# Kernel tuning notes

Measured on AMD Instinct MI355X. Metric: run time of the kernel, lower is better.

The kernel has to match this reference:

```python
import jax, jax.numpy as jnp
import numpy as np

B, K, D = 8, 256, 768      # batch, num proposals, appearance_feature_dim
DK = 96                    # key_feature_dim
DG = 96                    # geo_feature_dim
NR = 8                     # n_relations (NR*DK == D required by residual add)


def setup_inputs() -> dict:
    key = jax.random.key(0)
    ks = jax.random.split(key, 10)
    s = 0.02
    return {
        "f_a": jax.random.normal(ks[0], (B, K, D), jnp.float32),
        "position_embedding": jax.random.uniform(ks[1], (B, K, K, DG), jnp.float32),
        # stacked per-head parameters (NR heads)
        "WG_w": jax.random.normal(ks[2], (NR, DG), jnp.float32) * s,
        "WG_b": jnp.zeros((NR,), jnp.float32),
        "WK_w": jax.random.normal(ks[3], (NR, D, DK), jnp.float32) * s,
        "WK_b": jnp.zeros((NR, DK), jnp.float32),
        "WQ_w": jax.random.normal(ks[4], (NR, D, DK), jnp.float32) * s,
        "WQ_b": jnp.zeros((NR, DK), jnp.float32),
        "WV_w": jax.random.normal(ks[5], (NR, D, DK), jnp.float32) * s,
        "WV_b": jnp.zeros((NR, DK), jnp.float32),
    }


def reference(f_a, position_embedding, WG_w, WG_b, WK_w, WK_b, WQ_w, WQ_b, WV_w, WV_b):
    # Per-head projections, all heads at once: [B, H, K, DK]
    k = jnp.einsum('bkd,hde->bhke', f_a, WK_w) + WK_b[:, None, :]
    q = jnp.einsum('bkd,hde->bhke', f_a, WQ_w) + WQ_b[:, None, :]
    v = jnp.einsum('bkd,hde->bhke', f_a, WV_w) + WV_b[:, None, :]
    # scaled_dot[b,h,m,n] = <k_m, q_n> / sqrt(DK)  (matches w_k.view(B,K,1,dk)*w_q.view(B,1,K,dk))
    scores = jnp.einsum('bhme,bhne->bhmn', k, q) * (1.0 / np.sqrt(DK)).astype(np.float32)
    # geometric bias: relu(WG(pe)) -> [B,H,K,K]
    w_g = jax.nn.relu(jnp.einsum('bmng,hg->bhmn', position_embedding, WG_w) + WG_b[:, None, None])
    logits = jnp.log(jnp.clip(w_g, 1e-6)) + scores
    # torch Softmax(dim=1) on [B,K,K] -> normalize over m axis (axis=2 here)
    attn = jax.nn.softmax(logits, axis=2)
    # output[b,n,:] = sum_m attn[b,h,m,n] * v[b,h,m,:], heads concatenated on feature dim
    out = jnp.einsum('bhmn,bhmd->bnhd', attn, v).reshape(f_a.shape[0], f_a.shape[1], -1)
    return out + f_a  # concat + f_a residual from RelationalProposalModule
```

## Files before the change

kernel.cpp:

```cpp
#include <hip/hip_runtime.h>

#define DD   768
#define NH   8
#define DKh  96

typedef __attribute__((ext_vector_type(8))) short short8;
typedef __attribute__((ext_vector_type(4))) float f32x4;

__device__ __forceinline__ unsigned short f2bf(float x) {
    union { float f; unsigned int u; } v; v.f = x;
    unsigned int r = v.u + 0x7FFFu + ((v.u >> 16) & 1u);
    return (unsigned short)(r >> 16);
}

__global__ __launch_bounds__(256) void k_cvt_a(const float* __restrict__ fa,
                                               unsigned short* __restrict__ abf) {
    int idx = blockIdx.x * 256 + threadIdx.x;
    float4 v = ((const float4*)fa)[idx];
    ushort4 o;
    o.x = f2bf(v.x); o.y = f2bf(v.y); o.z = f2bf(v.z); o.w = f2bf(v.w);
    ((ushort4*)abf)[idx] = o;
}

__global__ __launch_bounds__(256) void k_cvt_w(const float* __restrict__ wk,
                                               const float* __restrict__ wq,
                                               const float* __restrict__ wv,
                                               unsigned short* __restrict__ wbf) {
    __shared__ float ls[64 * 97];
    int pid = blockIdx.x / 12;
    int db  = blockIdx.x % 12;
    int p = pid >> 3, h = pid & 7;
    const float* src = (p == 0 ? wk : p == 1 ? wq : wv) + h * DD * DKh + db * 64 * DKh;
    int t = threadIdx.x;
#pragma unroll
    for (int i = 0; i < 24; ++i) {
        int f = t + 256 * i;
        int dl = f / 96, e = f - dl * 96;
        ls[dl * 97 + e] = src[f];
    }
    __syncthreads();
    unsigned short* dst = wbf + (p * 768 + h * 96) * DD + db * 64;
#pragma unroll
    for (int i = 0; i < 24; ++i) {
        int f = t + 256 * i;
        int e = f >> 6, dl = f & 63;
        dst[e * DD + dl] = f2bf(ls[dl * 97 + e]);
    }
}

__global__ __launch_bounds__(256) void k_proj(const unsigned short* __restrict__ abf,
                                              const unsigned short* __restrict__ wbf,
                                              const float* __restrict__ wkb,
                                              const float* __restrict__ wqb,
                                              const float* __restrict__ wvb,
                                              unsigned short* __restrict__ kb,
                                              unsigned short* __restrict__ qb,
                                              unsigned short* __restrict__ vt) {
    int w = threadIdx.x >> 6, lane = threadIdx.x & 63;
    int lrow = lane & 15, quad = lane >> 4;
    int rt = blockIdx.x / 36, cg = blockIdx.x % 36;
    int r0 = rt * 64 + w * 16;
    int c0 = cg * 64;
    f32x4 z = {0.f, 0.f, 0.f, 0.f};
    f32x4 acc[4] = {z, z, z, z};
    for (int kk = 0; kk < DD; kk += 32) {
        short8 a = *(const short8*)(abf + (r0 + lrow) * DD + kk + quad * 8);
#pragma unroll
        for (int tt = 0; tt < 4; ++tt) {
            short8 b = *(const short8*)(wbf + (c0 + tt * 16 + lrow) * DD + kk + quad * 8);
            acc[tt] = __builtin_amdgcn_mfma_f32_16x16x32_bf16(a, b, acc[tt], 0, 0, 0);
        }
    }
    int rbase = r0 + quad * 4;
    int b_ = rbase >> 8, mbase = rbase & 255;
#pragma unroll
    for (int tt = 0; tt < 4; ++tt) {
        int cc = c0 + tt * 16 + lrow;
        int p = cc / 768, rm = cc - p * 768;
        int h = rm / 96,  e = rm - h * 96;
        float bias = (p == 0 ? wkb : p == 1 ? wqb : wvb)[h * 96 + e];
        if (p == 2) {
            ushort4 v4;
            v4.x = f2bf(acc[tt][0] + bias);
            v4.y = f2bf(acc[tt][1] + bias);
            v4.z = f2bf(acc[tt][2] + bias);
            v4.w = f2bf(acc[tt][3] + bias);
            *(ushort4*)(vt + ((b_ * 8 + h) * 96 + e) * 256 + mbase) = v4;
        } else {
            float sc = (p == 1) ? 0.10206207261596577f : 1.0f;
            unsigned short* dst = (p == 0 ? kb : qb) + ((b_ * 8 + h) * 256 + mbase) * 96 + e;
#pragma unroll
            for (int r = 0; r < 4; ++r)
                dst[r * 96] = f2bf((acc[tt][r] + bias) * sc);
        }
    }
}

__global__ __launch_bounds__(256) void k_wgs(const float* __restrict__ pe,
                                             const float* __restrict__ wgw,
                                             const float* __restrict__ wgb,
                                             const unsigned short* __restrict__ kb,
                                             const unsigned short* __restrict__ qb,
                                             float* __restrict__ L) {
    __shared__ unsigned short peb[256 * 96];
    __shared__ unsigned short wgl[16 * 96];
    __shared__ float stot[8 * 256];
    int bi = blockIdx.x;
    int b = bi >> 8, mt = (bi >> 4) & 15, nt = bi & 15;
    int m0 = mt * 16, n0 = nt * 16;
    int t = threadIdx.x;
#pragma unroll
    for (int i = 0; i < 6; ++i) {
        int f = t + 256 * i;
        int c = f / 96, k = f - c * 96;
        wgl[f] = (c < 8) ? f2bf(wgw[c * 96 + k]) : (unsigned short)0;
    }
    const float* peg = pe + ((size_t)(b * 256 + m0) * 256 + n0) * 96;
#pragma unroll
    for (int i = 0; i < 24; ++i) {
        int f = t + 256 * i;
        int mi = f / 384, rem = f - mi * 384;
        float4 v = *(const float4*)(peg + (size_t)mi * 24576 + rem * 4);
        ushort4 o;
        o.x = f2bf(v.x); o.y = f2bf(v.y); o.z = f2bf(v.z); o.w = f2bf(v.w);
        *(ushort4*)(peb + mi * 1536 + rem * 4) = o;
    }
    __syncthreads();
    int w = t >> 6, lane = t & 63, lrow = lane & 15, quad = lane >> 4;
    short8 bf[3];
#pragma unroll
    for (int ks = 0; ks < 3; ++ks)
        bf[ks] = *(const short8*)(wgl + lrow * 96 + ks * 32 + quad * 8);
    float gbias = wgb[lrow & 7];
#pragma unroll
    for (int rt4 = 0; rt4 < 4; ++rt4) {
        int rt = w * 4 + rt4;
        f32x4 acc = {0.f, 0.f, 0.f, 0.f};
#pragma unroll
        for (int ks = 0; ks < 3; ++ks) {
            short8 a = *(const short8*)(peb + (rt * 16 + lrow) * 96 + ks * 32 + quad * 8);
            acc = __builtin_amdgcn_mfma_f32_16x16x32_bf16(a, bf[ks], acc, 0, 0, 0);
        }
        if (lrow < 8) {
#pragma unroll
            for (int r = 0; r < 4; ++r)
                stot[lrow * 256 + rt * 16 + quad * 4 + r] =
                    __logf(fmaxf(acc[r] + gbias, 1e-6f));
        }
    }
    __syncthreads();
#pragma unroll
    for (int hh = 0; hh < 2; ++hh) {
        int h = w * 2 + hh;
        const unsigned short* ka = kb + ((size_t)((b * 8 + h) * 256) + m0 + lrow) * 96 + quad * 8;
        const unsigned short* qa = qb + ((size_t)((b * 8 + h) * 256) + n0 + lrow) * 96 + quad * 8;
        f32x4 acc = {0.f, 0.f, 0.f, 0.f};
#pragma unroll
        for (int ks = 0; ks < 3; ++ks) {
            short8 a  = *(const short8*)(ka + ks * 32);
            short8 bq = *(const short8*)(qa + ks * 32);
            acc = __builtin_amdgcn_mfma_f32_16x16x32_bf16(a, bq, acc, 0, 0, 0);
        }
        float* lp = L + ((size_t)((b * 8 + h) * 256) + m0 + quad * 4) * 256 + n0 + lrow;
#pragma unroll
        for (int r = 0; r < 4; ++r)
            lp[r * 256] = acc[r] + stot[h * 256 + (quad * 4 + r) * 16 + lrow];
    }
}

__global__ __launch_bounds__(256) void k_softmax(const float* __restrict__ L,
                                                 unsigned short* __restrict__ pt) {
    __shared__ float Ps[32 * 264];
    __shared__ float inv_s[32];
    int bh = blockIdx.x >> 3, nbk = blockIdx.x & 7;
    int n0 = nbk * 32;
    int t = threadIdx.x;
    int nl = t >> 3, j = t & 7;
    const float* base = L + bh * 65536 + n0 + nl;
    float mx = -3.4e38f;
    for (int m0 = 0; m0 < 256; m0 += 8)
        mx = fmaxf(mx, base[(m0 + j) * 256]);
    mx = fmaxf(mx, __shfl_xor(mx, 1));
    mx = fmaxf(mx, __shfl_xor(mx, 2));
    mx = fmaxf(mx, __shfl_xor(mx, 4));
    float sum = 0.f;
    for (int m0 = 0; m0 < 256; m0 += 8) {
        float v = base[(m0 + j) * 256];
        float e = __expf(v - mx);
        sum += e;
        Ps[nl * 264 + m0 + j] = e;
    }
    sum += __shfl_xor(sum, 1);
    sum += __shfl_xor(sum, 2);
    sum += __shfl_xor(sum, 4);
    if (j == 0) inv_s[nl] = 1.0f / sum;
    __syncthreads();
    unsigned short* dst = pt + (bh * 256 + n0) * 256;
#pragma unroll 4
    for (int i = 0; i < 32; ++i)
        dst[i * 256 + t] = f2bf(Ps[i * 264 + t] * inv_s[i]);
}

__global__ __launch_bounds__(256) void k_attnv(const unsigned short* __restrict__ pt,
                                               const unsigned short* __restrict__ vt,
                                               const float* __restrict__ fa,
                                               float* __restrict__ out) {
    int w = threadIdx.x >> 6, lane = threadIdx.x & 63;
    int lrow = lane & 15, quad = lane >> 4;
    int tid = blockIdx.x * 4 + w;
    int bh = tid / 96, rem = tid - bh * 96;
    int nt = rem / 6, et = rem - nt * 6;
    int n0 = nt * 16, e0 = et * 16;
    int b_ = bh >> 3, h = bh & 7;
    f32x4 acc = {0.f, 0.f, 0.f, 0.f};
    const unsigned short* pa = pt + (bh * 256 + n0 + lrow) * 256 + quad * 8;
    const unsigned short* va = vt + (bh * 96 + e0 + lrow) * 256 + quad * 8;
#pragma unroll
    for (int mk = 0; mk < 256; mk += 32) {
        short8 a = *(const short8*)(pa + mk);
        short8 b = *(const short8*)(va + mk);
        acc = __builtin_amdgcn_mfma_f32_16x16x32_bf16(a, b, acc, 0, 0, 0);
    }
    int idx = (b_ * 256 + n0 + quad * 4) * 768 + h * 96 + e0 + lrow;
#pragma unroll
    for (int r = 0; r < 4; ++r)
        out[idx + r * 768] = acc[r] + fa[idx + r * 768];
}

extern "C" void kernel_launch(void* const* d_in, const int* in_sizes, int n_in,
                              void* d_out, int out_size, void* d_ws, size_t ws_size,
                              hipStream_t stream) {
    const float* fa  = (const float*)d_in[0];
    const float* pe  = (const float*)d_in[1];
    const float* wgw = (const float*)d_in[2];
    const float* wgb = (const float*)d_in[3];
    const float* wkw = (const float*)d_in[4];
    const float* wkb = (const float*)d_in[5];
    const float* wqw = (const float*)d_in[6];
    const float* wqb = (const float*)d_in[7];
    const float* wvw = (const float*)d_in[8];
    const float* wvb = (const float*)d_in[9];
    float* out = (float*)d_out;
    char* ws = (char*)d_ws;
    unsigned short* abf = (unsigned short*)(ws);
    unsigned short* wbf = (unsigned short*)(ws + 3145728);
    unsigned short* kb  = (unsigned short*)(ws + 6684672);
    unsigned short* qb  = (unsigned short*)(ws + 9830400);
    unsigned short* vt  = (unsigned short*)(ws + 12976128);
    float*          L   = (float*)(ws + 16121856);
    unsigned short* pt  = (unsigned short*)(ws + 32899072);

    k_cvt_a  <<<1536, 256, 0, stream>>>(fa, abf);
    k_cvt_w  <<< 288, 256, 0, stream>>>(wkw, wqw, wvw, wbf);
    k_proj   <<<1152, 256, 0, stream>>>(abf, wbf, wkb, wqb, wvb, kb, qb, vt);
    k_wgs    <<<2048, 256, 0, stream>>>(pe, wgw, wgb, kb, qb, L);
    k_softmax<<< 512, 256, 0, stream>>>(L, pt);
    k_attnv  <<<1536, 256, 0, stream>>>(pt, vt, fa, out);
}
```

Baseline: 404.7 us.

## Fuse softmax with attn-V, transpose logits layout, merge conversion kernels

The two conversion kernels are merged into one launch. k_wgs now writes the logits transposed (n-major, m contiguous) with vectorized float4 stores, so the softmax over m becomes a contiguous row reduction using wave shuffles. Softmax and the attention-times-V product are fused into one kernel that keeps normalized probabilities in LDS as bf16, removing the pt round trip through global memory and two launches. The fused kernel launches only 512 blocks, which may lower parallelism in the matmul phase.

After: 390.7 us. -3.4%, faster.

```diff
diff --git a/kernel.cpp b/kernel.cpp
--- a/kernel.cpp
+++ b/kernel.cpp
@@ -13,25 +13,28 @@
     return (unsigned short)(r >> 16);
 }
 
-__global__ __launch_bounds__(256) void k_cvt_a(const float* __restrict__ fa,
-                                               unsigned short* __restrict__ abf) {
-    int idx = blockIdx.x * 256 + threadIdx.x;
-    float4 v = ((const float4*)fa)[idx];
-    ushort4 o;
-    o.x = f2bf(v.x); o.y = f2bf(v.y); o.z = f2bf(v.z); o.w = f2bf(v.w);
-    ((ushort4*)abf)[idx] = o;
-}
-
-__global__ __launch_bounds__(256) void k_cvt_w(const float* __restrict__ wk,
-                                               const float* __restrict__ wq,
-                                               const float* __restrict__ wv,
-                                               unsigned short* __restrict__ wbf) {
+__global__ __launch_bounds__(256) void k_cvt(const float* __restrict__ fa,
+                                             unsigned short* __restrict__ abf,
+                                             const float* __restrict__ wk,
+                                             const float* __restrict__ wq,
+                                             const float* __restrict__ wv,
+                                             unsigned short* __restrict__ wbf) {
     __shared__ float ls[64 * 97];
-    int pid = blockIdx.x / 12;
-    int db  = blockIdx.x % 12;
+    int bid = blockIdx.x;
+    int t = threadIdx.x;
+    if (bid < 1536) {
+        int idx = bid * 256 + t;
+        float4 v = ((const float4*)fa)[idx];
+        ushort4 o;
+        o.x = f2bf(v.x); o.y = f2bf(v.y); o.z = f2bf(v.z); o.w = f2bf(v.w);
+        ((ushort4*)abf)[idx] = o;
+        return;
+    }
+    int wb = bid - 1536;
+    int pid = wb / 12;
+    int db  = wb % 12;
     int p = pid >> 3, h = pid & 7;
     const float* src = (p == 0 ? wk : p == 1 ? wq : wv) + h * DD * DKh + db * 64 * DKh;
-    int t = threadIdx.x;
 #pragma unroll
     for (int i = 0; i < 24; ++i) {
         int f = t + 256 * i;
@@ -101,7 +104,7 @@
                                              const float* __restrict__ wgb,
                                              const unsigned short* __restrict__ kb,
                                              const unsigned short* __restrict__ qb,
-                                             float* __restrict__ L) {
+                                             float* __restrict__ Lt) {
     __shared__ unsigned short peb[256 * 96];
     __shared__ unsigned short wgl[16 * 96];
     __shared__ float stot[8 * 256];
@@ -161,70 +164,66 @@
             short8 bq = *(const short8*)(qa + ks * 32);
             acc = __builtin_amdgcn_mfma_f32_16x16x32_bf16(a, bq, acc, 0, 0, 0);
         }
-        float* lp = L + ((size_t)((b * 8 + h) * 256) + m0 + quad * 4) * 256 + n0 + lrow;
+        f32x4 ov;
 #pragma unroll
         for (int r = 0; r < 4; ++r)
-            lp[r * 256] = acc[r] + stot[h * 256 + (quad * 4 + r) * 16 + lrow];
-    }
-}
-
-__global__ __launch_bounds__(256) void k_softmax(const float* __restrict__ L,
-                                                 unsigned short* __restrict__ pt) {
-    __shared__ float Ps[32 * 264];
-    __shared__ float inv_s[32];
-    int bh = blockIdx.x >> 3, nbk = blockIdx.x & 7;
-    int n0 = nbk * 32;
-    int t = threadIdx.x;
-    int nl = t >> 3, j = t & 7;
-    const float* base = L + bh * 65536 + n0 + nl;
-    float mx = -3.4e38f;
-    for (int m0 = 0; m0 < 256; m0 += 8)
-        mx = fmaxf(mx, base[(m0 + j) * 256]);
-    mx = fmaxf(mx, __shfl_xor(mx, 1));
-    mx = fmaxf(mx, __shfl_xor(mx, 2));
-    mx = fmaxf(mx, __shfl_xor(mx, 4));
-    float sum = 0.f;
-    for (int m0 = 0; m0 < 256; m0 += 8) {
-        float v = base[(m0 + j) * 256];
-        float e = __expf(v - mx);
-        sum += e;
-        Ps[nl * 264 + m0 + j] = e;
-    }
-    sum += __shfl_xor(sum, 1);
-    sum += __shfl_xor(sum, 2);
-    sum += __shfl_xor(sum, 4);
-    if (j == 0) inv_s[nl] = 1.0f / sum;
-    __syncthreads();
-    unsigned short* dst = pt + (bh * 256 + n0) * 256;
-#pragma unroll 4
-    for (int i = 0; i < 32; ++i)
-        dst[i * 256 + t] = f2bf(Ps[i * 264 + t] * inv_s[i]);
-}
-
-__global__ __launch_bounds__(256) void k_attnv(const unsigned short* __restrict__ pt,
-                                               const unsigned short* __restrict__ vt,
-                                               const float* __restrict__ fa,
-                                               float* __restrict__ out) {
-    int w = threadIdx.x >> 6, lane = threadIdx.x & 63;
+            ov[r] = acc[r] + stot[h * 256 + (quad * 4 + r) * 16 + lrow];
+        *(f32x4*)(Lt + ((size_t)((b * 8 + h) * 256) + n0 + lrow) * 256 + m0 + quad * 4) = ov;
+    }
+}
+
+__global__ __launch_bounds__(256) void k_smv(const float* __restrict__ Lt,
+                                             const unsigned short* __restrict__ vt,
+                                             const float* __restrict__ fa,
+                                             float* __restrict__ out) {
+    __shared__ unsigned short P[32 * 264];
+    int bid = blockIdx.x;
+    int bh = bid >> 3, nt = bid & 7;
+    int n0 = nt * 32;
+    int t = threadIdx.x, w = t >> 6, lane = t & 63;
+    const float* lb = Lt + ((size_t)bh * 256 + n0) * 256;
+#pragma unroll
+    for (int rr = 0; rr < 8; ++rr) {
+        int row = w * 8 + rr;
+        float4 v = *((const float4*)(lb + row * 256) + lane);
+        float mx = fmaxf(fmaxf(v.x, v.y), fmaxf(v.z, v.w));
+#pragma unroll
+        for (int d = 1; d < 64; d <<= 1) mx = fmaxf(mx, __shfl_xor(mx, d));
+        float e0 = __expf(v.x - mx), e1 = __expf(v.y - mx),
+              e2 = __expf(v.z - mx), e3 = __expf(v.w - mx);
+        float s = e0 + e1 + e2 + e3;
+#pragma unroll
+        for (int d = 1; d < 64; d <<= 1) s += __shfl_xor(s, d);
+        float inv = 1.0f / s;
+        ushort4 o;
+        o.x = f2bf(e0 * inv); o.y = f2bf(e1 * inv);
+        o.z = f2bf(e2 * inv); o.w = f2bf(e3 * inv);
+        *(ushort4*)(P + row * 264 + lane * 4) = o;
+    }
+    __syncthreads();
     int lrow = lane & 15, quad = lane >> 4;
-    int tid = blockIdx.x * 4 + w;
-    int bh = tid / 96, rem = tid - bh * 96;
-    int nt = rem / 6, et = rem - nt * 6;
-    int n0 = nt * 16, e0 = et * 16;
+    int nsub = (w & 1) * 16, eb = (w >> 1) * 48;
+    f32x4 zz = {0.f, 0.f, 0.f, 0.f};
+    f32x4 acc[3] = {zz, zz, zz};
+    const unsigned short* vb = vt + ((size_t)bh * 96 + eb + lrow) * 256 + quad * 8;
+    const unsigned short* pb = P + (nsub + lrow) * 264 + quad * 8;
+#pragma unroll
+    for (int mk = 0; mk < 256; mk += 32) {
+        short8 a = *(const short8*)(pb + mk);
+#pragma unroll
+        for (int tt = 0; tt < 3; ++tt) {
+            short8 b = *(const short8*)(vb + tt * 16 * 256 + mk);
+            acc[tt] = __builtin_amdgcn_mfma_f32_16x16x32_bf16(a, b, acc[tt], 0, 0, 0);
+        }
+    }
     int b_ = bh >> 3, h = bh & 7;
-    f32x4 acc = {0.f, 0.f, 0.f, 0.f};
-    const unsigned short* pa = pt + (bh * 256 + n0 + lrow) * 256 + quad * 8;
-    const unsigned short* va = vt + (bh * 96 + e0 + lrow) * 256 + quad * 8;
-#pragma unroll
-    for (int mk = 0; mk < 256; mk += 32) {
-        short8 a = *(const short8*)(pa + mk);
-        short8 b = *(const short8*)(va + mk);
-        acc = __builtin_amdgcn_mfma_f32_16x16x32_bf16(a, b, acc, 0, 0, 0);
-    }
-    int idx = (b_ * 256 + n0 + quad * 4) * 768 + h * 96 + e0 + lrow;
-#pragma unroll
-    for (int r = 0; r < 4; ++r)
-        out[idx + r * 768] = acc[r] + fa[idx + r * 768];
+#pragma unroll
+    for (int tt = 0; tt < 3; ++tt) {
+        int idx = (b_ * 256 + n0 + nsub + quad * 4) * 768 + h * 96 + eb + tt * 16 + lrow;
+#pragma unroll
+        for (int r = 0; r < 4; ++r)
+            out[idx + r * 768] = acc[tt][r] + fa[idx + r * 768];
+    }
 }
 
 extern "C" void kernel_launch(void* const* d_in, const int* in_sizes, int n_in,
@@ -247,13 +246,10 @@
     unsigned short* kb  = (unsigned short*)(ws + 6684672);
     unsigned short* qb  = (unsigned short*)(ws + 9830400);
     unsigned short* vt  = (unsigned short*)(ws + 12976128);
-    float*          L   = (float*)(ws + 16121856);
-    unsigned short* pt  = (unsigned short*)(ws + 32899072);
-
-    k_cvt_a  <<<1536, 256, 0, stream>>>(fa, abf);
-    k_cvt_w  <<< 288, 256, 0, stream>>>(wkw, wqw, wvw, wbf);
-    k_proj   <<<1152, 256, 0, stream>>>(abf, wbf, wkb, wqb, wvb, kb, qb, vt);
-    k_wgs    <<<2048, 256, 0, stream>>>(pe, wgw, wgb, kb, qb, L);
-    k_softmax<<< 512, 256, 0, stream>>>(L, pt);
-    k_attnv  <<<1536, 256, 0, stream>>>(pt, vt, fa, out);
-}
+    float*          Lt  = (float*)(ws + 16121856);
+
+    k_cvt <<<1824, 256, 0, stream>>>(fa, abf, wkw, wqw, wvw, wbf);
+    k_proj<<<1152, 256, 0, stream>>>(abf, wbf, wkb, wqb, wvb, kb, qb, vt);
+    k_wgs <<<2048, 256, 0, stream>>>(pe, wgw, wgb, kb, qb, Lt);
+    k_smv <<< 512, 256, 0, stream>>>(Lt, vt, fa, out);
+}
```
